# Optimization experiments

Hardware: AMD Instinct MI355X
Metric: run time of the kernel (lower is better)

Reference implementation:

```python
import jax, jax.numpy as jnp
import numpy as np

N = 50000   # num_nodes
E = 800000  # num_edges
IN, HID, OUT = 64, 96, 96
LN_EPS = 1e-5


def setup_inputs() -> dict:
    key = jax.random.key(0)
    ks = jax.random.split(key, 12)
    s = 0.05
    return {
        "x": jax.random.normal(ks[0], (N, IN), jnp.float32),
        "edge_index": jax.random.randint(ks[1], (2, E), 0, N, dtype=jnp.int64),
        "edge_weight": jax.random.uniform(ks[2], (E,), jnp.float32),
        "W0": jax.random.normal(ks[3], (IN, HID), jnp.float32) * s,
        "b0": jnp.zeros((HID,), jnp.float32),
        "ln_g": jnp.ones((HID,), jnp.float32),
        "ln_b": jnp.zeros((HID,), jnp.float32),
        "Ws": jax.random.normal(ks[4], (IN, HID), jnp.float32) * s,
        "bs": jnp.zeros((HID,), jnp.float32),
        "W1": jax.random.normal(ks[5], (HID, OUT), jnp.float32) * s,
        "b1": jnp.zeros((OUT,), jnp.float32),
    }


def _gcn(h, W, b, src, dst, ew, n):
    # GCNConv with add_self_loops=True and edge weights (PyG gcn_norm)
    loop = jnp.arange(n, dtype=src.dtype)
    s = jnp.concatenate([src, loop])
    d = jnp.concatenate([dst, loop])
    w = jnp.concatenate([ew, jnp.ones((n,), ew.dtype)])
    deg = jax.ops.segment_sum(w, d, num_segments=n)
    dinv = jnp.where(deg > 0, jax.lax.rsqrt(jnp.maximum(deg, 1e-12)), 0.0)
    norm = dinv[s] * w * dinv[d]                 # [E+N]
    msg = (h @ W)[s] * norm[:, None]             # gather transformed src feats
    return jax.ops.segment_sum(msg, d, num_segments=n) + b


def _layernorm(h, g, b):
    mu = h.mean(-1, keepdims=True)
    var = ((h - mu) ** 2).mean(-1, keepdims=True)
    return (h - mu) * jax.lax.rsqrt(var + LN_EPS) * g + b


def reference(x, edge_index, edge_weight, W0, b0, ln_g, ln_b, Ws, bs, W1, b1):
    src, dst = edge_index[0], edge_index[1]
    n = x.shape[0]
    # layer 0: GCN -> LayerNorm -> ReLU -> (dropout: eval no-op) -> +Linear skip
    h = _gcn(x, W0, b0, src, dst, edge_weight, n)
    h = jax.nn.relu(_layernorm(h, ln_g, ln_b))
    h = h + (x @ Ws + bs)
    # final layer: GCN only
    return _gcn(h, W1, b1, src, dst, edge_weight, n)
```

## Files before the change

kernel.cpp:

```cpp
#include <hip/hip_runtime.h>

#define LN_EPS 1e-5f

__device__ __forceinline__ float bflo(unsigned u) { union { unsigned u; float f; } c; c.u = u << 16; return c.f; }
__device__ __forceinline__ float bfhi(unsigned u) { union { unsigned u; float f; } c; c.u = u & 0xffff0000u; return c.f; }
__device__ __forceinline__ unsigned f2bfbits(float f) {
    union { float f; unsigned u; } c; c.f = f;
    return (c.u + 0x7fffu + ((c.u >> 16) & 1u)) >> 16;
}
__device__ __forceinline__ unsigned packbf(float lo, float hi) {
    return f2bfbits(lo) | (f2bfbits(hi) << 16);
}

__global__ void init_kernel(int* __restrict__ cnt, int n) {
    int i = blockIdx.x * 256 + threadIdx.x;
    if (i < n) cnt[i] = 0;
}

__global__ void cnt_kernel(const int* __restrict__ dst, int* __restrict__ cnt, int e) {
    int i = blockIdx.x * 256 + threadIdx.x;
    if (i >= e) return;
    atomicAdd(&cnt[dst[i]], 1);
}

__global__ void cvt_x_kernel(const float* __restrict__ x, unsigned* __restrict__ xb2, int total4) {
    int i = blockIdx.x * 256 + threadIdx.x;
    if (i >= total4) return;
    float4 v = ((const float4*)x)[i];
    uint2 o;
    o.x = packbf(v.x, v.y);
    o.y = packbf(v.z, v.w);
    ((uint2*)xb2)[i] = o;
}

__global__ void prep_w_kernel(const float* __restrict__ W0, const float* __restrict__ Ws,
                              const float* __restrict__ W1,
                              float4* __restrict__ w0i, float4* __restrict__ wsi,
                              float4* __restrict__ w1i) {
    int i = blockIdx.x * 256 + threadIdx.x;
    if (i < 1536) {
        int kq = i / 96, j = i % 96;
        const float* p = W0 + kq * 4 * 96 + j;
        w0i[i] = make_float4(p[0], p[96], p[192], p[288]);
        const float* q = Ws + kq * 4 * 96 + j;
        wsi[i] = make_float4(q[0], q[96], q[192], q[288]);
    }
    int i2 = i - 1536;
    if (i2 >= 0 && i2 < 2304) {
        int kq = i2 / 96, j = i2 % 96;
        const float* p = W1 + kq * 4 * 96 + j;
        w1i[i2] = make_float4(p[0], p[96], p[192], p[288]);
    }
}

__global__ void blocksum_kernel(const int* __restrict__ cnt, int* __restrict__ bsum, int n) {
    int base = blockIdx.x * 1024;
    int t = threadIdx.x;
    int i0 = base + t * 4;
    int s = 0;
    if (i0 + 3 < n) { int4 v = *(const int4*)(cnt + i0); s = v.x + v.y + v.z + v.w; }
    else { for (int k = 0; k < 4; ++k) if (i0 + k < n) s += cnt[i0 + k]; }
    #pragma unroll
    for (int off = 32; off; off >>= 1) s += __shfl_xor(s, off);
    __shared__ int wsum[4];
    if ((t & 63) == 0) wsum[t >> 6] = s;
    __syncthreads();
    if (t == 0) bsum[blockIdx.x] = wsum[0] + wsum[1] + wsum[2] + wsum[3];
}

__global__ void scan_bsum_kernel(const int* __restrict__ bsum, int* __restrict__ boff, int nb) {
    int t = threadIdx.x;
    int carry = 0;
    for (int base = 0; base < nb; base += 64) {
        int i = base + t;
        int v = (i < nb) ? bsum[i] : 0;
        int sc = v;
        #pragma unroll
        for (int off = 1; off < 64; off <<= 1) {
            int u = __shfl_up(sc, off);
            if (t >= off) sc += u;
        }
        if (i < nb) boff[i] = carry + sc - v;
        carry += __shfl(sc, 63);
    }
}

__global__ void rowptr_kernel(const int* __restrict__ cnt, const int* __restrict__ boff,
                              int* __restrict__ rowptr, int* __restrict__ rowcur,
                              int n, int etot) {
    __shared__ int wsum[4];
    int b = blockIdx.x;
    int t = threadIdx.x;
    int i0 = b * 1024 + t * 4;
    int c0 = 0, c1 = 0, c2 = 0, c3 = 0;
    if (i0 < n)     c0 = cnt[i0];
    if (i0 + 1 < n) c1 = cnt[i0 + 1];
    if (i0 + 2 < n) c2 = cnt[i0 + 2];
    if (i0 + 3 < n) c3 = cnt[i0 + 3];
    int tot = c0 + c1 + c2 + c3;
    int lane = t & 63, w = t >> 6;
    int sc = tot;
    #pragma unroll
    for (int off = 1; off < 64; off <<= 1) {
        int u = __shfl_up(sc, off);
        if (lane >= off) sc += u;
    }
    if (lane == 63) wsum[w] = sc;
    __syncthreads();
    int woff = 0;
    for (int k = 0; k < w; ++k) woff += wsum[k];
    int excl = boff[b] + woff + sc - tot;
    if (i0 < n)     { rowptr[i0]     = excl;             rowcur[i0]     = excl; }
    if (i0 + 1 < n) { rowptr[i0 + 1] = excl + c0;        rowcur[i0 + 1] = excl + c0; }
    if (i0 + 2 < n) { rowptr[i0 + 2] = excl + c0 + c1;   rowcur[i0 + 2] = excl + c0 + c1; }
    if (i0 + 3 < n) { rowptr[i0 + 3] = excl + c0 + c1 + c2; rowcur[i0 + 3] = excl + c0 + c1 + c2; }
    if (b == 0 && t == 0) rowptr[n] = etot;
}

__global__ void scatter_kernel(const int* __restrict__ src, const int* __restrict__ dst,
                               const float* __restrict__ ew,
                               int* __restrict__ rowcur,
                               int* __restrict__ col, float* __restrict__ val, int e) {
    int i = blockIdx.x * 256 + threadIdx.x;
    if (i >= e) return;
    int s = src[i], d = dst[i];
    int pos = atomicAdd(&rowcur[d], 1);
    col[pos] = s;
    val[pos] = ew[i];
}

__global__ void degsum_kernel(const int* __restrict__ rowptr, const float* __restrict__ val,
                              float* __restrict__ dinv, int n) {
    int i = blockIdx.x * 256 + threadIdx.x;
    if (i >= n) return;
    int p0 = rowptr[i], p1 = rowptr[i + 1];
    float s = 1.0f;
    for (int p = p0; p < p1; ++p) s += val[p];
    dinv[i] = rsqrtf(s);
}

__global__ void rescale_kernel(const int* __restrict__ col, const float* __restrict__ dinv,
                               float* __restrict__ val, int e) {
    int i = blockIdx.x * 256 + threadIdx.x;
    if (i >= e) return;
    val[i] *= dinv[col[i]];
}

__global__ void agg64_kernel(const unsigned* __restrict__ xb, const float* __restrict__ dinv,
                             const int* __restrict__ rowptr, const int* __restrict__ col,
                             const float* __restrict__ val, float* __restrict__ aggX, int n) {
    int node = blockIdx.x * 4 + (threadIdx.x >> 6);
    if (node >= n) return;
    int lane = threadIdx.x & 63;
    int g = lane >> 4, l4 = lane & 15;
    const uint2* x2 = (const uint2*)xb;
    int p0 = rowptr[node], pe = rowptr[node + 1];
    float a0 = 0, a1 = 0, a2 = 0, a3 = 0;
    float b0 = 0, b1 = 0, b2 = 0, b3 = 0;
    for (int p = p0 + g; p < pe; p += 8) {
        int s1 = col[p]; float w1 = val[p];
        uint2 r1 = x2[(size_t)s1 * 16 + l4];
        bool h2 = (p + 4) < pe;
        int s2 = h2 ? col[p + 4] : s1;
        float w2 = h2 ? val[p + 4] : 0.0f;
        uint2 r2 = x2[(size_t)s2 * 16 + l4];
        a0 = fmaf(w1, bflo(r1.x), a0); a1 = fmaf(w1, bfhi(r1.x), a1);
        a2 = fmaf(w1, bflo(r1.y), a2); a3 = fmaf(w1, bfhi(r1.y), a3);
        b0 = fmaf(w2, bflo(r2.x), b0); b1 = fmaf(w2, bfhi(r2.x), b1);
        b2 = fmaf(w2, bflo(r2.y), b2); b3 = fmaf(w2, bfhi(r2.y), b3);
    }
    a0 += b0; a1 += b1; a2 += b2; a3 += b3;
    #pragma unroll
    for (int off = 16; off <= 32; off <<= 1) {
        a0 += __shfl_xor(a0, off);
        a1 += __shfl_xor(a1, off);
        a2 += __shfl_xor(a2, off);
        a3 += __shfl_xor(a3, off);
    }
    if (g == 0) {
        float di = dinv[node];
        uint2 sr = x2[(size_t)node * 16 + l4];
        a0 = fmaf(di, bflo(sr.x), a0); a1 = fmaf(di, bfhi(sr.x), a1);
        a2 = fmaf(di, bflo(sr.y), a2); a3 = fmaf(di, bfhi(sr.y), a3);
        ((float4*)(aggX + (size_t)node * 64))[l4] =
            make_float4(a0 * di, a1 * di, a2 * di, a3 * di);
    }
}

__global__ __launch_bounds__(512) void gemm_ln_kernel(
        const float4* __restrict__ w0i, const float4* __restrict__ wsi,
        const float* __restrict__ aggX, const float* __restrict__ x,
        const float* __restrict__ b0,
        const float* __restrict__ ln_g, const float* __restrict__ ln_b,
        const float* __restrict__ bs,
        unsigned short* __restrict__ hb, int n) {
    __shared__ float4 w0s[1536];
    __shared__ float4 wss[1536];
    __shared__ float4 ar[1024];
    __shared__ float4 xr[1024];
    int t = threadIdx.x;
    int base = blockIdx.x * 64;
    for (int i = t; i < 1536; i += 512) { w0s[i] = w0i[i]; wss[i] = wsi[i]; }
    int rem = n - base; if (rem > 64) rem = 64;
    int nf4 = rem * 16;
    for (int i = t; i < nf4; i += 512) {
        ar[i] = ((const float4*)(aggX + (size_t)base * 64))[i];
        xr[i] = ((const float4*)(x + (size_t)base * 64))[i];
    }
    __syncthreads();
    int hw = t >> 5;
    int l = t & 31;
    int r0 = hw * 4;
    float acc[4][3] = {{0.f,0.f,0.f},{0.f,0.f,0.f},{0.f,0.f,0.f},{0.f,0.f,0.f}};
    float sk[4][3]  = {{0.f,0.f,0.f},{0.f,0.f,0.f},{0.f,0.f,0.f},{0.f,0.f,0.f}};
    for (int kq = 0; kq < 16; ++kq) {
        float4 wa = w0s[kq * 96 + l];
        float4 wb = w0s[kq * 96 + l + 32];
        float4 wc = w0s[kq * 96 + l + 64];
        float4 sa = wss[kq * 96 + l];
        float4 sb = wss[kq * 96 + l + 32];
        float4 scv = wss[kq * 96 + l + 64];
        #pragma unroll
        for (int r = 0; r < 4; ++r) {
            float4 a  = ar[(r0 + r) * 16 + kq];
            float4 xv = xr[(r0 + r) * 16 + kq];
            acc[r][0] = fmaf(a.w, wa.w, fmaf(a.z, wa.z, fmaf(a.y, wa.y, fmaf(a.x, wa.x, acc[r][0]))));
            acc[r][1] = fmaf(a.w, wb.w, fmaf(a.z, wb.z, fmaf(a.y, wb.y, fmaf(a.x, wb.x, acc[r][1]))));
            acc[r][2] = fmaf(a.w, wc.w, fmaf(a.z, wc.z, fmaf(a.y, wc.y, fmaf(a.x, wc.x, acc[r][2]))));
            sk[r][0]  = fmaf(xv.w, sa.w, fmaf(xv.z, sa.z, fmaf(xv.y, sa.y, fmaf(xv.x, sa.x, sk[r][0]))));
            sk[r][1]  = fmaf(xv.w, sb.w, fmaf(xv.z, sb.z, fmaf(xv.y, sb.y, fmaf(xv.x, sb.x, sk[r][1]))));
            sk[r][2]  = fmaf(xv.w, scv.w, fmaf(xv.z, scv.z, fmaf(xv.y, scv.y, fmaf(xv.x, scv.x, sk[r][2]))));
        }
    }
    float b00 = b0[l], b01 = b0[l + 32], b02 = b0[l + 64];
    float g0 = ln_g[l], g1 = ln_g[l + 32], g2 = ln_g[l + 64];
    float e0 = ln_b[l], e1 = ln_b[l + 32], e2 = ln_b[l + 64];
    float q0 = bs[l],   q1 = bs[l + 32],   q2 = bs[l + 64];
    #pragma unroll
    for (int r = 0; r < 4; ++r) {
        int node = base + r0 + r;
        if (node >= n) break;
        float a0v = acc[r][0] + b00, a1v = acc[r][1] + b01, a2v = acc[r][2] + b02;
        float s1 = a0v + a1v + a2v;
        #pragma unroll
        for (int off = 1; off < 32; off <<= 1) s1 += __shfl_xor(s1, off);
        float mu = s1 * (1.0f / 96.0f);
        float d0 = a0v - mu, d1 = a1v - mu, d2 = a2v - mu;
        float sq = d0 * d0 + d1 * d1 + d2 * d2;
        #pragma unroll
        for (int off = 1; off < 32; off <<= 1) sq += __shfl_xor(sq, off);
        float rinv = rsqrtf(sq * (1.0f / 96.0f) + LN_EPS);
        float v0 = fmaxf(d0 * rinv * g0 + e0, 0.0f) + sk[r][0] + q0;
        float v1 = fmaxf(d1 * rinv * g1 + e1, 0.0f) + sk[r][1] + q1;
        float v2 = fmaxf(d2 * rinv * g2 + e2, 0.0f) + sk[r][2] + q2;
        unsigned short* o = hb + (size_t)node * 128;
        o[l]      = (unsigned short)f2bfbits(v0);
        o[l + 32] = (unsigned short)f2bfbits(v1);
        o[l + 64] = (unsigned short)f2bfbits(v2);
        o[l + 96] = 0;
    }
}

__global__ void agg96_kernel(const unsigned short* __restrict__ hb, const float* __restrict__ dinv,
                             const int* __restrict__ rowptr, const int* __restrict__ col,
                             const float* __restrict__ val, float* __restrict__ aggH, int n) {
    int node = blockIdx.x * 4 + (threadIdx.x >> 6);
    if (node >= n) return;
    int lane = threadIdx.x & 63;
    int g = lane >> 4, l4 = lane & 15;
    const uint4* h4 = (const uint4*)hb;
    int p0 = rowptr[node], pe = rowptr[node + 1];
    float a0=0,a1=0,a2=0,a3=0,a4=0,a5=0,a6=0,a7=0;
    float c0=0,c1=0,c2=0,c3=0,c4=0,c5=0,c6=0,c7=0;
    for (int p = p0 + g; p < pe; p += 8) {
        int s1 = col[p]; float w1 = val[p];
        uint4 r1 = h4[(size_t)s1 * 16 + l4];
        bool h2 = (p + 4) < pe;
        int s2 = h2 ? col[p + 4] : s1;
        float w2 = h2 ? val[p + 4] : 0.0f;
        uint4 r2 = h4[(size_t)s2 * 16 + l4];
        a0 = fmaf(w1, bflo(r1.x), a0); a1 = fmaf(w1, bfhi(r1.x), a1);
        a2 = fmaf(w1, bflo(r1.y), a2); a3 = fmaf(w1, bfhi(r1.y), a3);
        a4 = fmaf(w1, bflo(r1.z), a4); a5 = fmaf(w1, bfhi(r1.z), a5);
        a6 = fmaf(w1, bflo(r1.w), a6); a7 = fmaf(w1, bfhi(r1.w), a7);
        c0 = fmaf(w2, bflo(r2.x), c0); c1 = fmaf(w2, bfhi(r2.x), c1);
        c2 = fmaf(w2, bflo(r2.y), c2); c3 = fmaf(w2, bfhi(r2.y), c3);
        c4 = fmaf(w2, bflo(r2.z), c4); c5 = fmaf(w2, bfhi(r2.z), c5);
        c6 = fmaf(w2, bflo(r2.w), c6); c7 = fmaf(w2, bfhi(r2.w), c7);
    }
    a0+=c0; a1+=c1; a2+=c2; a3+=c3; a4+=c4; a5+=c5; a6+=c6; a7+=c7;
    #pragma unroll
    for (int off = 16; off <= 32; off <<= 1) {
        a0 += __shfl_xor(a0, off); a1 += __shfl_xor(a1, off);
        a2 += __shfl_xor(a2, off); a3 += __shfl_xor(a3, off);
        a4 += __shfl_xor(a4, off); a5 += __shfl_xor(a5, off);
        a6 += __shfl_xor(a6, off); a7 += __shfl_xor(a7, off);
    }
    if (g == 0 && l4 < 12) {
        float di = dinv[node];
        uint4 sr = h4[(size_t)node * 16 + l4];
        a0 = fmaf(di, bflo(sr.x), a0); a1 = fmaf(di, bfhi(sr.x), a1);
        a2 = fmaf(di, bflo(sr.y), a2); a3 = fmaf(di, bfhi(sr.y), a3);
        a4 = fmaf(di, bflo(sr.z), a4); a5 = fmaf(di, bfhi(sr.z), a5);
        a6 = fmaf(di, bflo(sr.w), a6); a7 = fmaf(di, bfhi(sr.w), a7);
        float4* o = (float4*)(aggH + (size_t)node * 96);
        o[l4 * 2]     = make_float4(a0 * di, a1 * di, a2 * di, a3 * di);
        o[l4 * 2 + 1] = make_float4(a4 * di, a5 * di, a6 * di, a7 * di);
    }
}

__global__ __launch_bounds__(512) void gemm_out_kernel(
        const float4* __restrict__ w1i, const float* __restrict__ aggH,
        const float* __restrict__ b1, float* __restrict__ out, int n) {
    __shared__ float4 w1s[2304];
    __shared__ float4 hr[1536];
    int t = threadIdx.x;
    int base = blockIdx.x * 64;
    for (int i = t; i < 2304; i += 512) w1s[i] = w1i[i];
    int rem = n - base; if (rem > 64) rem = 64;
    int nf4 = rem * 24;
    for (int i = t; i < nf4; i += 512)
        hr[i] = ((const float4*)(aggH + (size_t)base * 96))[i];
    __syncthreads();
    int hw = t >> 5, l = t & 31;
    int r0 = hw * 4;
    float acc[4][3] = {{0.f,0.f,0.f},{0.f,0.f,0.f},{0.f,0.f,0.f},{0.f,0.f,0.f}};
    for (int kq = 0; kq < 24; ++kq) {
        float4 wa = w1s[kq * 96 + l];
        float4 wb = w1s[kq * 96 + l + 32];
        float4 wc = w1s[kq * 96 + l + 64];
        #pragma unroll
        for (int r = 0; r < 4; ++r) {
            float4 a = hr[(r0 + r) * 24 + kq];
            acc[r][0] = fmaf(a.w, wa.w, fmaf(a.z, wa.z, fmaf(a.y, wa.y, fmaf(a.x, wa.x, acc[r][0]))));
            acc[r][1] = fmaf(a.w, wb.w, fmaf(a.z, wb.z, fmaf(a.y, wb.y, fmaf(a.x, wb.x, acc[r][1]))));
            acc[r][2] = fmaf(a.w, wc.w, fmaf(a.z, wc.z, fmaf(a.y, wc.y, fmaf(a.x, wc.x, acc[r][2]))));
        }
    }
    float c0 = b1[l], c1 = b1[l + 32], c2 = b1[l + 64];
    #pragma unroll
    for (int r = 0; r < 4; ++r) {
        int node = base + r0 + r;
        if (node >= n) break;
        float* o = out + (size_t)node * 96;
        o[l]      = acc[r][0] + c0;
        o[l + 32] = acc[r][1] + c1;
        o[l + 64] = acc[r][2] + c2;
    }
}

extern "C" void kernel_launch(void* const* d_in, const int* in_sizes, int n_in,
                              void* d_out, int out_size, void* d_ws, size_t ws_size,
                              hipStream_t stream) {
    const float* x    = (const float*)d_in[0];
    const int*   ei   = (const int*)d_in[1];
    const float* ew   = (const float*)d_in[2];
    const float* W0   = (const float*)d_in[3];
    const float* b0   = (const float*)d_in[4];
    const float* ln_g = (const float*)d_in[5];
    const float* ln_b = (const float*)d_in[6];
    const float* Ws   = (const float*)d_in[7];
    const float* bs   = (const float*)d_in[8];
    const float* W1   = (const float*)d_in[9];
    const float* b1   = (const float*)d_in[10];
    float* out = (float*)d_out;

    const int E = in_sizes[2];
    const int N = in_sizes[0] / 64;
    const int* src = ei;
    const int* dst = ei + E;

    char* ws = (char*)d_ws;
    size_t off = 0;
    auto alloc = [&](size_t bytes) -> void* {
        void* p = ws + off;
        off = (off + bytes + 255) & ~(size_t)255;
        return p;
    };
    float* dinv   = (float*)alloc((size_t)N * 4);
    int*   cnt    = (int*)alloc((size_t)N * 4);
    int*   rowptr = (int*)alloc((size_t)(N + 1) * 4);
    int*   rowcur = (int*)alloc((size_t)N * 4);
    int*   bsum   = (int*)alloc((size_t)256 * 4);
    int*   boff   = (int*)alloc((size_t)256 * 4);
    int*   col    = (int*)alloc((size_t)E * 4);
    float* val    = (float*)alloc((size_t)E * 4);
    unsigned* xb  = (unsigned*)alloc((size_t)N * 64 * 2);
    unsigned short* hb = (unsigned short*)alloc((size_t)N * 128 * 2);
    float* bufA   = (float*)alloc((size_t)N * 96 * 4);
    float4* w0i   = (float4*)alloc((size_t)1536 * 16);
    float4* wsi   = (float4*)alloc((size_t)1536 * 16);
    float4* w1i   = (float4*)alloc((size_t)2304 * 16);

    int gN = (N + 255) / 256;
    int gE = (E + 255) / 256;
    int nb = (N + 1023) / 1024;

    init_kernel<<<gN, 256, 0, stream>>>(cnt, N);
    cnt_kernel<<<gE, 256, 0, stream>>>(dst, cnt, E);
    cvt_x_kernel<<<(N * 16 + 255) / 256, 256, 0, stream>>>(x, xb, N * 16);
    prep_w_kernel<<<15, 256, 0, stream>>>(W0, Ws, W1, w0i, wsi, w1i);
    blocksum_kernel<<<nb, 256, 0, stream>>>(cnt, bsum, N);
    scan_bsum_kernel<<<1, 64, 0, stream>>>(bsum, boff, nb);
    rowptr_kernel<<<nb, 256, 0, stream>>>(cnt, boff, rowptr, rowcur, N, E);
    scatter_kernel<<<gE, 256, 0, stream>>>(src, dst, ew, rowcur, col, val, E);
    degsum_kernel<<<gN, 256, 0, stream>>>(rowptr, val, dinv, N);
    rescale_kernel<<<gE, 256, 0, stream>>>(col, dinv, val, E);

    int gA = (N + 3) / 4;
    agg64_kernel<<<gA, 256, 0, stream>>>(xb, dinv, rowptr, col, val, bufA, N);

    int gG = (N + 63) / 64;
    gemm_ln_kernel<<<gG, 512, 0, stream>>>(w0i, wsi, bufA, x, b0, ln_g, ln_b, bs, hb, N);

    agg96_kernel<<<gA, 256, 0, stream>>>(hb, dinv, rowptr, col, val, bufA, N);

    gemm_out_kernel<<<gG, 512, 0, stream>>>(w1i, bufA, b1, out, N);
}
```

Before: 240.5 us.

## Partition CSR count/scatter by destination range and interleave col/val into uint2

Count and scatter kernels now run as 8 groups of blocks. Each group scans all edges but only handles destinations in its own eighth of the node range, which localizes the atomics and random writes. The separate col and val arrays are merged into one interleaved uint2 array, so scatter, rescale and both aggregation kernels fetch index and weight with a single 8-byte load. The cost is reading dst eight times and running a fixed 1024-block grid.

```diff
diff --git a/kernel.cpp b/kernel.cpp
--- a/kernel.cpp
+++ b/kernel.cpp
@@ -17,10 +17,18 @@
     if (i < n) cnt[i] = 0;
 }
 
-__global__ void cnt_kernel(const int* __restrict__ dst, int* __restrict__ cnt, int e) {
-    int i = blockIdx.x * 256 + threadIdx.x;
-    if (i >= e) return;
-    atomicAdd(&cnt[dst[i]], 1);
+__global__ void cnt_part_kernel(const int* __restrict__ dst, int* __restrict__ cnt,
+                                int e, int n) {
+    int part = blockIdx.x & 7;
+    int blk  = blockIdx.x >> 3;
+    int chunk = (n + 7) >> 3;
+    int lo = part * chunk;
+    int hi = lo + chunk; if (hi > n) hi = n;
+    int stride = (gridDim.x >> 3) * 256;
+    for (int i = blk * 256 + threadIdx.x; i < e; i += stride) {
+        int d = dst[i];
+        if (d >= lo && d < hi) atomicAdd(&cnt[d], 1);
+    }
 }
 
 __global__ void cvt_x_kernel(const float* __restrict__ x, unsigned* __restrict__ xb2, int total4) {
@@ -117,38 +125,48 @@
     if (b == 0 && t == 0) rowptr[n] = etot;
 }
 
-__global__ void scatter_kernel(const int* __restrict__ src, const int* __restrict__ dst,
-                               const float* __restrict__ ew,
-                               int* __restrict__ rowcur,
-                               int* __restrict__ col, float* __restrict__ val, int e) {
-    int i = blockIdx.x * 256 + threadIdx.x;
-    if (i >= e) return;
-    int s = src[i], d = dst[i];
-    int pos = atomicAdd(&rowcur[d], 1);
-    col[pos] = s;
-    val[pos] = ew[i];
-}
-
-__global__ void degsum_kernel(const int* __restrict__ rowptr, const float* __restrict__ val,
+__global__ void scatter_part_kernel(const int* __restrict__ src, const int* __restrict__ dst,
+                                    const float* __restrict__ ew,
+                                    int* __restrict__ rowcur,
+                                    uint2* __restrict__ cv, int e, int n) {
+    int part = blockIdx.x & 7;
+    int blk  = blockIdx.x >> 3;
+    int chunk = (n + 7) >> 3;
+    int lo = part * chunk;
+    int hi = lo + chunk; if (hi > n) hi = n;
+    int stride = (gridDim.x >> 3) * 256;
+    for (int i = blk * 256 + threadIdx.x; i < e; i += stride) {
+        int d = dst[i];
+        if (d >= lo && d < hi) {
+            int s = src[i];
+            float w = ew[i];
+            int pos = atomicAdd(&rowcur[d], 1);
+            cv[pos] = make_uint2((unsigned)s, __float_as_uint(w));
+        }
+    }
+}
+
+__global__ void degsum_kernel(const int* __restrict__ rowptr, const uint2* __restrict__ cv,
                               float* __restrict__ dinv, int n) {
     int i = blockIdx.x * 256 + threadIdx.x;
     if (i >= n) return;
     int p0 = rowptr[i], p1 = rowptr[i + 1];
     float s = 1.0f;
-    for (int p = p0; p < p1; ++p) s += val[p];
+    for (int p = p0; p < p1; ++p) s += __uint_as_float(cv[p].y);
     dinv[i] = rsqrtf(s);
 }
 
-__global__ void rescale_kernel(const int* __restrict__ col, const float* __restrict__ dinv,
-                               float* __restrict__ val, int e) {
+__global__ void rescale_kernel(const float* __restrict__ dinv, uint2* __restrict__ cv, int e) {
     int i = blockIdx.x * 256 + threadIdx.x;
     if (i >= e) return;
-    val[i] *= dinv[col[i]];
+    uint2 v = cv[i];
+    v.y = __float_as_uint(__uint_as_float(v.y) * dinv[v.x]);
+    cv[i] = v;
 }
 
 __global__ void agg64_kernel(const unsigned* __restrict__ xb, const float* __restrict__ dinv,
-                             const int* __restrict__ rowptr, const int* __restrict__ col,
-                             const float* __restrict__ val, float* __restrict__ aggX, int n) {
+                             const int* __restrict__ rowptr, const uint2* __restrict__ cv,
+                             float* __restrict__ aggX, int n) {
     int node = blockIdx.x * 4 + (threadIdx.x >> 6);
     if (node >= n) return;
     int lane = threadIdx.x & 63;
@@ -158,11 +176,13 @@
     float a0 = 0, a1 = 0, a2 = 0, a3 = 0;
     float b0 = 0, b1 = 0, b2 = 0, b3 = 0;
     for (int p = p0 + g; p < pe; p += 8) {
-        int s1 = col[p]; float w1 = val[p];
+        uint2 e1 = cv[p];
+        int s1 = (int)e1.x; float w1 = __uint_as_float(e1.y);
         uint2 r1 = x2[(size_t)s1 * 16 + l4];
         bool h2 = (p + 4) < pe;
-        int s2 = h2 ? col[p + 4] : s1;
-        float w2 = h2 ? val[p + 4] : 0.0f;
+        uint2 e2 = h2 ? cv[p + 4] : e1;
+        int s2 = (int)e2.x;
+        float w2 = h2 ? __uint_as_float(e2.y) : 0.0f;
         uint2 r2 = x2[(size_t)s2 * 16 + l4];
         a0 = fmaf(w1, bflo(r1.x), a0); a1 = fmaf(w1, bfhi(r1.x), a1);
         a2 = fmaf(w1, bflo(r1.y), a2); a3 = fmaf(w1, bfhi(r1.y), a3);
@@ -262,8 +282,8 @@
 }
 
 __global__ void agg96_kernel(const unsigned short* __restrict__ hb, const float* __restrict__ dinv,
-                             const int* __restrict__ rowptr, const int* __restrict__ col,
-                             const float* __restrict__ val, float* __restrict__ aggH, int n) {
+                             const int* __restrict__ rowptr, const uint2* __restrict__ cv,
+                             float* __restrict__ aggH, int n) {
     int node = blockIdx.x * 4 + (threadIdx.x >> 6);
     if (node >= n) return;
     int lane = threadIdx.x & 63;
@@ -273,11 +293,13 @@
     float a0=0,a1=0,a2=0,a3=0,a4=0,a5=0,a6=0,a7=0;
     float c0=0,c1=0,c2=0,c3=0,c4=0,c5=0,c6=0,c7=0;
     for (int p = p0 + g; p < pe; p += 8) {
-        int s1 = col[p]; float w1 = val[p];
+        uint2 e1 = cv[p];
+        int s1 = (int)e1.x; float w1 = __uint_as_float(e1.y);
         uint4 r1 = h4[(size_t)s1 * 16 + l4];
         bool h2 = (p + 4) < pe;
-        int s2 = h2 ? col[p + 4] : s1;
-        float w2 = h2 ? val[p + 4] : 0.0f;
+        uint2 e2 = h2 ? cv[p + 4] : e1;
+        int s2 = (int)e2.x;
+        float w2 = h2 ? __uint_as_float(e2.y) : 0.0f;
         uint4 r2 = h4[(size_t)s2 * 16 + l4];
         a0 = fmaf(w1, bflo(r1.x), a0); a1 = fmaf(w1, bfhi(r1.x), a1);
         a2 = fmaf(w1, bflo(r1.y), a2); a3 = fmaf(w1, bfhi(r1.y), a3);
@@ -383,8 +405,7 @@
     int*   rowcur = (int*)alloc((size_t)N * 4);
     int*   bsum   = (int*)alloc((size_t)256 * 4);
     int*   boff   = (int*)alloc((size_t)256 * 4);
-    int*   col    = (int*)alloc((size_t)E * 4);
-    float* val    = (float*)alloc((size_t)E * 4);
+    uint2* cv     = (uint2*)alloc((size_t)E * 8);
     unsigned* xb  = (unsigned*)alloc((size_t)N * 64 * 2);
     unsigned short* hb = (unsigned short*)alloc((size_t)N * 128 * 2);
     float* bufA   = (float*)alloc((size_t)N * 96 * 4);
@@ -395,25 +416,26 @@
     int gN = (N + 255) / 256;
     int gE = (E + 255) / 256;
     int nb = (N + 1023) / 1024;
+    int gP = 8 * 128;
 
     init_kernel<<<gN, 256, 0, stream>>>(cnt, N);
-    cnt_kernel<<<gE, 256, 0, stream>>>(dst, cnt, E);
+    cnt_part_kernel<<<gP, 256, 0, stream>>>(dst, cnt, E, N);
     cvt_x_kernel<<<(N * 16 + 255) / 256, 256, 0, stream>>>(x, xb, N * 16);
     prep_w_kernel<<<15, 256, 0, stream>>>(W0, Ws, W1, w0i, wsi, w1i);
     blocksum_kernel<<<nb, 256, 0, stream>>>(cnt, bsum, N);
     scan_bsum_kernel<<<1, 64, 0, stream>>>(bsum, boff, nb);
     rowptr_kernel<<<nb, 256, 0, stream>>>(cnt, boff, rowptr, rowcur, N, E);
-    scatter_kernel<<<gE, 256, 0, stream>>>(src, dst, ew, rowcur, col, val, E);
-    degsum_kernel<<<gN, 256, 0, stream>>>(rowptr, val, dinv, N);
-    rescale_kernel<<<gE, 256, 0, stream>>>(col, dinv, val, E);
+    scatter_part_kernel<<<gP, 256, 0, stream>>>(src, dst, ew, rowcur, cv, E, N);
+    degsum_kernel<<<gN, 256, 0, stream>>>(rowptr, cv, dinv, N);
+    rescale_kernel<<<gE, 256, 0, stream>>>(dinv, cv, E);
 
     int gA = (N + 3) / 4;
-    agg64_kernel<<<gA, 256, 0, stream>>>(xb, dinv, rowptr, col, val, bufA, N);
+    agg64_kernel<<<gA, 256, 0, stream>>>(xb, dinv, rowptr, cv, bufA, N);
 
     int gG = (N + 63) / 64;
     gemm_ln_kernel<<<gG, 512, 0, stream>>>(w0i, wsi, bufA, x, b0, ln_g, ln_b, bs, hb, N);
 
-    agg96_kernel<<<gA, 256, 0, stream>>>(hb, dinv, rowptr, col, val, bufA, N);
+    agg96_kernel<<<gA, 256, 0, stream>>>(hb, dinv, rowptr, cv, bufA, N);
 
     gemm_out_kernel<<<gG, 512, 0, stream>>>(w1i, bufA, b1, out, N);
 }
```

Result: no change. 239.1 us (-0.6%).
